# Kernel optimization log

Hardware: AMD Instinct MI355X
Metric: run time of the kernel (lower is better)

The kernel has to match this reference:

```python
import jax, jax.numpy as jnp
import numpy as np

NEG_SLOPE = 0.01  # F.leaky_relu default used in the original forward


def setup_inputs() -> dict:
    key = jax.random.key(0)
    ks = jax.random.split(key, 6)
    B, N, D = 2, 4096, 128
    s = 1.0 / np.sqrt(D)
    return {
        "embed_feat": jax.random.normal(ks[0], (B, N, D), jnp.float32),
        "predict_G": 1,
        "W_demand": jax.random.normal(ks[1], (D,), jnp.float32) * s,
        "b_demand": jnp.zeros((1,), jnp.float32),
        "Wa": jax.random.normal(ks[2], (D, D), jnp.float32) * s,
        "w_l": jax.random.normal(ks[3], (D,), jnp.float32) * s,
        "w_r": jax.random.normal(ks[4], (D,), jnp.float32) * s,
    }


def reference(embed_feat, predict_G, W_demand, b_demand, Wa, w_l, w_r):
    # demands: sigmoid(Linear(D->1)) -> [B, N]
    demands = jax.nn.sigmoid(embed_feat @ W_demand + b_demand[0])
    if not predict_G:
        return (demands, None)
    # proj = Wa(x): [B, N, D]  (torch Linear: x @ Wa.T)
    proj = jnp.einsum('bnd,ed->bne', embed_feat, Wa)
    # per-node scalar scores; A[b,i,j] = l[b,i] + r[b,j] (vectorized form of the O(N^2) loop)
    l = proj @ w_l  # [B, N]
    r = proj @ w_r  # [B, N]
    A = jax.nn.leaky_relu(l[:, :, None] + r[:, None, :], negative_slope=NEG_SLOPE)
    # original softmax over dim=1 of [N, N, 1] == over j axis
    Q = jax.nn.softmax(A, axis=2)  # [B, N, N]
    # rel_Ds[b,i,j] = demands[b,i]
    Gs = Q * demands[:, :, None]
    return (demands, Gs)
```

## Files before the change

kernel.cpp:

```cpp
#include <hip/hip_runtime.h>
#include <stdint.h>

#define N 4096
#define B 2
#define D 128
#define LOG2E 1.4426950408889634f

__device__ __forceinline__ float lrelu(float t) { return t > 0.f ? t : 0.01f * t; }

__global__ __launch_bounds__(256) void k1_uvec(
    const float* __restrict__ Wa,
    const float* __restrict__ w_l,
    const float* __restrict__ w_r,
    float* __restrict__ u) {
    __shared__ float2 pl[4][64];
    __shared__ float2 pr[4][64];
    int t = threadIdx.x;
    int d2 = t & 63;
    int h = t >> 6;
    const float2* Wa2 = (const float2*)Wa;
    float2 al = make_float2(0.f, 0.f), ar = make_float2(0.f, 0.f);
    #pragma unroll 8
    for (int k = 0; k < 32; ++k) {
        int e = h * 32 + k;
        float2 w = Wa2[e * 64 + d2];
        float wl = w_l[e];
        float wr = w_r[e];
        al.x += w.x * wl; al.y += w.y * wl;
        ar.x += w.x * wr; ar.y += w.y * wr;
    }
    pl[h][d2] = al; pr[h][d2] = ar;
    __syncthreads();
    if (t < 64) {
        float2 s = make_float2(0.f, 0.f);
        #pragma unroll
        for (int hh = 0; hh < 4; ++hh) { s.x += pl[hh][t].x; s.y += pl[hh][t].y; }
        ((float2*)u)[t] = s;
    } else if (t < 128) {
        int dd = t - 64;
        float2 s = make_float2(0.f, 0.f);
        #pragma unroll
        for (int hh = 0; hh < 4; ++hh) { s.x += pr[hh][dd].x; s.y += pr[hh][dd].y; }
        ((float2*)(u + D))[dd] = s;
    }
}

__global__ __launch_bounds__(256) void k2_rows(
    const float* __restrict__ x,
    const float* __restrict__ Wd,
    const float* __restrict__ bd,
    const float* __restrict__ u,
    float* __restrict__ out_dem,
    float* __restrict__ lv,
    float* __restrict__ rv) {
    int lane = threadIdx.x & 63;
    int row = blockIdx.x * 4 + (threadIdx.x >> 6);
    float2 xv = ((const float2*)(x + (size_t)row * D))[lane];
    float2 ul2 = ((const float2*)u)[lane];
    float2 ur2 = ((const float2*)(u + D))[lane];
    float2 wv = ((const float2*)Wd)[lane];
    float pl = xv.x * ul2.x + xv.y * ul2.y;
    float pr = xv.x * ur2.x + xv.y * ur2.y;
    float pd = xv.x * wv.x + xv.y * wv.y;
    #pragma unroll
    for (int m = 32; m >= 1; m >>= 1) {
        pl += __shfl_xor(pl, m, 64);
        pr += __shfl_xor(pr, m, 64);
        pd += __shfl_xor(pd, m, 64);
    }
    if (lane == 0) {
        float dem = 1.f / (1.f + __expf(-(pd + bd[0])));
        out_dem[row] = dem;
        lv[row] = pl * LOG2E;
        rv[row] = pr * LOG2E;
    }
}

__global__ __launch_bounds__(256) void k3_main(
    const float* __restrict__ lv, const float* __restrict__ rv,
    const float* __restrict__ dem_f,
    float* __restrict__ out_g) {
    __shared__ float sr[N];
    __shared__ float redmax[4];
    __shared__ float redsum[4][4];
    int tid = threadIdx.x;
    int b = blockIdx.x >> 10;
    int i0 = (blockIdx.x & 1023) << 2;
    const float* rb = rv + b * N;
    float lmax = -3.402823466e38f;
    #pragma unroll
    for (int k = 0; k < N / 256; ++k) {
        float v = rb[tid + k * 256];
        sr[tid + k * 256] = v;
        lmax = fmaxf(lmax, v);
    }
    #pragma unroll
    for (int m = 32; m >= 1; m >>= 1) lmax = fmaxf(lmax, __shfl_xor(lmax, m, 64));
    if ((tid & 63) == 0) redmax[tid >> 6] = lmax;
    __syncthreads();
    float rmax = fmaxf(fmaxf(redmax[0], redmax[1]), fmaxf(redmax[2], redmax[3]));

    int rowbase = b * N + i0;
    float lr_[4], mr[4], s[4];
    #pragma unroll
    for (int q = 0; q < 4; ++q) {
        lr_[q] = lv[rowbase + q];
        mr[q] = lrelu(lr_[q] + rmax);
        s[q] = 0.f;
    }
    #pragma unroll 2
    for (int k = 0; k < N / 256; ++k) {
        float r = sr[tid + k * 256];
        #pragma unroll
        for (int q = 0; q < 4; ++q) s[q] += exp2f(lrelu(lr_[q] + r) - mr[q]);
    }
    #pragma unroll
    for (int m = 32; m >= 1; m >>= 1) {
        #pragma unroll
        for (int q = 0; q < 4; ++q) s[q] += __shfl_xor(s[q], m, 64);
    }
    if ((tid & 63) == 0) {
        #pragma unroll
        for (int q = 0; q < 4; ++q) redsum[tid >> 6][q] = s[q];
    }
    __syncthreads();
    float sc[4];
    #pragma unroll
    for (int q = 0; q < 4; ++q) {
        float den = redsum[0][q] + redsum[1][q] + redsum[2][q] + redsum[3][q];
        sc[q] = dem_f[rowbase + q] / den;
    }
    const float4* rb4 = (const float4*)rb;
    size_t gbase = (size_t)b * N * N + (size_t)i0 * N;
    #pragma unroll
    for (int it = 0; it < 4; ++it) {
        int idx = it * 256 + tid;
        float4 r4 = rb4[idx];
        #pragma unroll
        for (int q = 0; q < 4; ++q) {
            float4 o;
            o.x = exp2f(lrelu(lr_[q] + r4.x) - mr[q]) * sc[q];
            o.y = exp2f(lrelu(lr_[q] + r4.y) - mr[q]) * sc[q];
            o.z = exp2f(lrelu(lr_[q] + r4.z) - mr[q]) * sc[q];
            o.w = exp2f(lrelu(lr_[q] + r4.w) - mr[q]) * sc[q];
            *(float4*)(out_g + gbase + (size_t)q * N + (size_t)idx * 4) = o;
        }
    }
}

extern "C" void kernel_launch(void* const* d_in, const int* in_sizes, int n_in,
                              void* d_out, int out_size, void* d_ws, size_t ws_size,
                              hipStream_t stream) {
    const float* x  = (const float*)d_in[0];
    const float* Wd = (const float*)d_in[2];
    const float* bd = (const float*)d_in[3];
    const float* Wa = (const float*)d_in[4];
    const float* wl = (const float*)d_in[5];
    const float* wr = (const float*)d_in[6];

    float* ws = (float*)d_ws;
    float* u  = ws;
    float* lv = ws + 256;
    float* rv = ws + 256 + 8192;

    float* out     = (float*)d_out;
    float* out_dem = out;
    float* out_g   = out + B * N;

    hipLaunchKernelGGL(k1_uvec, dim3(1), dim3(256), 0, stream, Wa, wl, wr, u);
    hipLaunchKernelGGL(k2_rows, dim3(B * N / 4), dim3(256), 0, stream,
                       x, Wd, bd, u, out_dem, lv, rv);
    hipLaunchKernelGGL(k3_main, dim3(B * N / 4), dim3(256), 0, stream,
                       lv, rv, out_dem, out_g);
}
```

Baseline: 155.7 us.

## Factor softmax exponentials into per-column precomputed terms and global max

The leaky-relu softmax exponent is split into exp2(l+r) for positive and exp2(0.01(l+r)) for negative arguments, each factored into a per-row scale times a per-column term. A new kernel precomputes exp2(r-rmax) and exp2(0.01(r-rmax)) per column, and the per-batch max of r is found once with an ordered-integer atomicMax instead of in every block. The main kernel then needs only compares, selects and multiplies with no per-element exp2, and its stores are nontemporal. The costs are an extra launch, four times more column data read per block, and possible overflow or precision loss when the factored terms are far from the max.

```diff
diff --git a/kernel.cpp b/kernel.cpp
--- a/kernel.cpp
+++ b/kernel.cpp
@@ -6,16 +6,28 @@
 #define D 128
 #define LOG2E 1.4426950408889634f
 
+typedef float f32x4 __attribute__((ext_vector_type(4)));
+
 __device__ __forceinline__ float lrelu(float t) { return t > 0.f ? t : 0.01f * t; }
+
+__device__ __forceinline__ unsigned f2ord(float f) {
+    unsigned u = __float_as_uint(f);
+    return (u & 0x80000000u) ? ~u : (u | 0x80000000u);
+}
+__device__ __forceinline__ float ord2f(unsigned o) {
+    return __uint_as_float((o & 0x80000000u) ? (o ^ 0x80000000u) : ~o);
+}
 
 __global__ __launch_bounds__(256) void k1_uvec(
     const float* __restrict__ Wa,
     const float* __restrict__ w_l,
     const float* __restrict__ w_r,
-    float* __restrict__ u) {
+    float* __restrict__ u,
+    unsigned* __restrict__ gmax) {
     __shared__ float2 pl[4][64];
     __shared__ float2 pr[4][64];
     int t = threadIdx.x;
+    if (t < B) gmax[t] = 0u;
     int d2 = t & 63;
     int h = t >> 6;
     const float2* Wa2 = (const float2*)Wa;
@@ -52,7 +64,8 @@
     const float* __restrict__ u,
     float* __restrict__ out_dem,
     float* __restrict__ lv,
-    float* __restrict__ rv) {
+    float4* __restrict__ q4,
+    unsigned* __restrict__ gmax) {
     int lane = threadIdx.x & 63;
     int row = blockIdx.x * 4 + (threadIdx.x >> 6);
     float2 xv = ((const float2*)(x + (size_t)row * D))[lane];
@@ -72,78 +85,95 @@
         float dem = 1.f / (1.f + __expf(-(pd + bd[0])));
         out_dem[row] = dem;
         lv[row] = pl * LOG2E;
-        rv[row] = pr * LOG2E;
-    }
+        float r = pr * LOG2E;
+        q4[row].x = r;
+        atomicMax(gmax + (row >> 12), f2ord(r));
+    }
+}
+
+__global__ __launch_bounds__(256) void k2b_fpm(
+    float4* __restrict__ q4,
+    const unsigned* __restrict__ gmax) {
+    int j = blockIdx.x * 256 + threadIdx.x;
+    float rmax = ord2f(gmax[j >> 12]);
+    float r = q4[j].x;
+    float t = r - rmax;
+    q4[j] = make_float4(r, exp2f(t), exp2f(0.01f * t), 0.f);
 }
 
 __global__ __launch_bounds__(256) void k3_main(
-    const float* __restrict__ lv, const float* __restrict__ rv,
+    const float* __restrict__ lv,
+    const float4* __restrict__ q4,
+    const unsigned* __restrict__ gmax,
     const float* __restrict__ dem_f,
     float* __restrict__ out_g) {
-    __shared__ float sr[N];
-    __shared__ float redmax[4];
-    __shared__ float redsum[4][4];
+    __shared__ float red[4][8];
     int tid = threadIdx.x;
     int b = blockIdx.x >> 10;
     int i0 = (blockIdx.x & 1023) << 2;
-    const float* rb = rv + b * N;
-    float lmax = -3.402823466e38f;
-    #pragma unroll
+    const float4* qb = q4 + (size_t)b * N;
+    float rmax = ord2f(gmax[b]);
+    int rowbase = b * N + i0;
+
+    float l_[4];
+    #pragma unroll
+    for (int q = 0; q < 4; ++q) l_[q] = lv[rowbase + q];
+
+    float s1[4] = {0.f, 0.f, 0.f, 0.f}, s2[4] = {0.f, 0.f, 0.f, 0.f};
+    #pragma unroll 4
     for (int k = 0; k < N / 256; ++k) {
-        float v = rb[tid + k * 256];
-        sr[tid + k * 256] = v;
-        lmax = fmaxf(lmax, v);
-    }
-    #pragma unroll
-    for (int m = 32; m >= 1; m >>= 1) lmax = fmaxf(lmax, __shfl_xor(lmax, m, 64));
-    if ((tid & 63) == 0) redmax[tid >> 6] = lmax;
+        float4 v = qb[tid + k * 256];
+        #pragma unroll
+        for (int q = 0; q < 4; ++q) {
+            bool pos = (l_[q] + v.x) > 0.f;
+            s1[q] += pos ? v.y : 0.f;
+            s2[q] += pos ? 0.f : v.z;
+        }
+    }
+    #pragma unroll
+    for (int m = 32; m >= 1; m >>= 1) {
+        #pragma unroll
+        for (int q = 0; q < 4; ++q) {
+            s1[q] += __shfl_xor(s1[q], m, 64);
+            s2[q] += __shfl_xor(s2[q], m, 64);
+        }
+    }
+    int w = tid >> 6;
+    if ((tid & 63) == 0) {
+        #pragma unroll
+        for (int q = 0; q < 4; ++q) { red[w][q] = s1[q]; red[w][4 + q] = s2[q]; }
+    }
     __syncthreads();
-    float rmax = fmaxf(fmaxf(redmax[0], redmax[1]), fmaxf(redmax[2], redmax[3]));
-
-    int rowbase = b * N + i0;
-    float lr_[4], mr[4], s[4];
+    float eP[4], eM[4];
     #pragma unroll
     for (int q = 0; q < 4; ++q) {
-        lr_[q] = lv[rowbase + q];
-        mr[q] = lrelu(lr_[q] + rmax);
-        s[q] = 0.f;
-    }
-    #pragma unroll 2
-    for (int k = 0; k < N / 256; ++k) {
-        float r = sr[tid + k * 256];
-        #pragma unroll
-        for (int q = 0; q < 4; ++q) s[q] += exp2f(lrelu(lr_[q] + r) - mr[q]);
-    }
-    #pragma unroll
-    for (int m = 32; m >= 1; m >>= 1) {
-        #pragma unroll
-        for (int q = 0; q < 4; ++q) s[q] += __shfl_xor(s[q], m, 64);
-    }
-    if ((tid & 63) == 0) {
-        #pragma unroll
-        for (int q = 0; q < 4; ++q) redsum[tid >> 6][q] = s[q];
-    }
-    __syncthreads();
-    float sc[4];
-    #pragma unroll
-    for (int q = 0; q < 4; ++q) {
-        float den = redsum[0][q] + redsum[1][q] + redsum[2][q] + redsum[3][q];
-        sc[q] = dem_f[rowbase + q] / den;
-    }
-    const float4* rb4 = (const float4*)rb;
+        float S1 = red[0][q] + red[1][q] + red[2][q] + red[3][q];
+        float S2 = red[0][4 + q] + red[1][4 + q] + red[2][4 + q] + red[3][4 + q];
+        float t0 = l_[q] + rmax;
+        float m0 = lrelu(t0);
+        float Ep = exp2f(t0 - m0);
+        float Em = exp2f(0.01f * t0 - m0);
+        float sc = dem_f[rowbase + q] / (Ep * S1 + Em * S2);
+        eP[q] = Ep * sc;
+        eM[q] = Em * sc;
+    }
+
     size_t gbase = (size_t)b * N * N + (size_t)i0 * N;
     #pragma unroll
     for (int it = 0; it < 4; ++it) {
         int idx = it * 256 + tid;
-        float4 r4 = rb4[idx];
+        float4 v0 = qb[idx * 4 + 0];
+        float4 v1 = qb[idx * 4 + 1];
+        float4 v2 = qb[idx * 4 + 2];
+        float4 v3 = qb[idx * 4 + 3];
         #pragma unroll
         for (int q = 0; q < 4; ++q) {
-            float4 o;
-            o.x = exp2f(lrelu(lr_[q] + r4.x) - mr[q]) * sc[q];
-            o.y = exp2f(lrelu(lr_[q] + r4.y) - mr[q]) * sc[q];
-            o.z = exp2f(lrelu(lr_[q] + r4.z) - mr[q]) * sc[q];
-            o.w = exp2f(lrelu(lr_[q] + r4.w) - mr[q]) * sc[q];
-            *(float4*)(out_g + gbase + (size_t)q * N + (size_t)idx * 4) = o;
+            f32x4 o;
+            o.x = (l_[q] + v0.x > 0.f) ? eP[q] * v0.y : eM[q] * v0.z;
+            o.y = (l_[q] + v1.x > 0.f) ? eP[q] * v1.y : eM[q] * v1.z;
+            o.z = (l_[q] + v2.x > 0.f) ? eP[q] * v2.y : eM[q] * v2.z;
+            o.w = (l_[q] + v3.x > 0.f) ? eP[q] * v3.y : eM[q] * v3.z;
+            __builtin_nontemporal_store(o, (f32x4*)(out_g + gbase + (size_t)q * N) + idx);
         }
     }
 }
@@ -161,15 +191,17 @@
     float* ws = (float*)d_ws;
     float* u  = ws;
     float* lv = ws + 256;
-    float* rv = ws + 256 + 8192;
+    float4* q4 = (float4*)(ws + 256 + 8192);
+    unsigned* gmax = (unsigned*)(ws + 256 + 8192 + 4 * 8192);
 
     float* out     = (float*)d_out;
     float* out_dem = out;
     float* out_g   = out + B * N;
 
-    hipLaunchKernelGGL(k1_uvec, dim3(1), dim3(256), 0, stream, Wa, wl, wr, u);
+    hipLaunchKernelGGL(k1_uvec, dim3(1), dim3(256), 0, stream, Wa, wl, wr, u, gmax);
     hipLaunchKernelGGL(k2_rows, dim3(B * N / 4), dim3(256), 0, stream,
-                       x, Wd, bd, u, out_dem, lv, rv);
+                       x, Wd, bd, u, out_dem, lv, q4, gmax);
+    hipLaunchKernelGGL(k2b_fpm, dim3(B * N / 256), dim3(256), 0, stream, q4, gmax);
     hipLaunchKernelGGL(k3_main, dim3(B * N / 4), dim3(256), 0, stream,
-                       lv, rv, out_dem, out_g);
-}
+                       lv, q4, gmax, out_dem, out_g);
+}
```

After: 259.4 us. +66.5%, slower.

## Fuse all stages into one cooperative kernel with factored leaky-relu exponentials

Applied to the files above, without the earlier changes.

Merges the three kernels into one cooperative launch of 512 blocks with a grid-wide sync between the per-row projection stage and the softmax stage. Each block now handles 16 rows instead of 4, and every block recomputes the tiny Wa·w vectors itself. The exp2 of leaky_relu(l+r) is factored into per-column tables exp2(r-rmax) and exp2(0.01(r-rmax)) held in LDS, selected per element by a threshold compare. This removes the per-element transcendental from the output loop. The cost is a grid sync, redundant per-block Wa work, a register-heavy 16-row store loop, and dependence on cooperative-launch residency.

```diff
diff --git a/kernel.cpp b/kernel.cpp
--- a/kernel.cpp
+++ b/kernel.cpp
@@ -1,149 +1,167 @@
 #include <hip/hip_runtime.h>
+#include <hip/hip_cooperative_groups.h>
 #include <stdint.h>
+
+namespace cg = cooperative_groups;
 
 #define N 4096
 #define B 2
 #define D 128
 #define LOG2E 1.4426950408889634f
 
+typedef float f32x4 __attribute__((ext_vector_type(4)));
+
 __device__ __forceinline__ float lrelu(float t) { return t > 0.f ? t : 0.01f * t; }
 
-__global__ __launch_bounds__(256) void k1_uvec(
+__global__ __launch_bounds__(256, 2) void kfused(
+    const float* __restrict__ x,
+    const float* __restrict__ Wd,
+    const float* __restrict__ bd,
     const float* __restrict__ Wa,
     const float* __restrict__ w_l,
     const float* __restrict__ w_r,
-    float* __restrict__ u) {
-    __shared__ float2 pl[4][64];
-    __shared__ float2 pr[4][64];
+    float* __restrict__ colR,
+    float* __restrict__ out_dem,
+    float* __restrict__ out_g) {
+    __shared__ float sFp[N];
+    __shared__ float sFm[N];
+    __shared__ float uLR[2][D];
+    __shared__ float sWd[D];
+    __shared__ float redm[4];
+    __shared__ float4 rowfacS[16];
+
     int t = threadIdx.x;
-    int d2 = t & 63;
-    int h = t >> 6;
-    const float2* Wa2 = (const float2*)Wa;
-    float2 al = make_float2(0.f, 0.f), ar = make_float2(0.f, 0.f);
-    #pragma unroll 8
-    for (int k = 0; k < 32; ++k) {
-        int e = h * 32 + k;
-        float2 w = Wa2[e * 64 + d2];
-        float wl = w_l[e];
-        float wr = w_r[e];
-        al.x += w.x * wl; al.y += w.y * wl;
-        ar.x += w.x * wr; ar.y += w.y * wr;
-    }
-    pl[h][d2] = al; pr[h][d2] = ar;
-    __syncthreads();
-    if (t < 64) {
-        float2 s = make_float2(0.f, 0.f);
-        #pragma unroll
-        for (int hh = 0; hh < 4; ++hh) { s.x += pl[hh][t].x; s.y += pl[hh][t].y; }
-        ((float2*)u)[t] = s;
-    } else if (t < 128) {
-        int dd = t - 64;
-        float2 s = make_float2(0.f, 0.f);
-        #pragma unroll
-        for (int hh = 0; hh < 4; ++hh) { s.x += pr[hh][dd].x; s.y += pr[hh][dd].y; }
-        ((float2*)(u + D))[dd] = s;
-    }
-}
+    int lane = t & 63;
+    int w = t >> 6;
+    int bk = blockIdx.x;
+    int row0 = bk << 4;
+    int b = bk >> 8;
 
-__global__ __launch_bounds__(256) void k2_rows(
-    const float* __restrict__ x,
-    const float* __restrict__ Wd,
-    const float* __restrict__ bd,
-    const float* __restrict__ u,
-    float* __restrict__ out_dem,
-    float* __restrict__ lv,
-    float* __restrict__ rv) {
-    int lane = threadIdx.x & 63;
-    int row = blockIdx.x * 4 + (threadIdx.x >> 6);
-    float2 xv = ((const float2*)(x + (size_t)row * D))[lane];
-    float2 ul2 = ((const float2*)u)[lane];
-    float2 ur2 = ((const float2*)(u + D))[lane];
-    float2 wv = ((const float2*)Wd)[lane];
-    float pl = xv.x * ul2.x + xv.y * ul2.y;
-    float pr = xv.x * ur2.x + xv.y * ur2.y;
-    float pd = xv.x * wv.x + xv.y * wv.y;
-    #pragma unroll
-    for (int m = 32; m >= 1; m >>= 1) {
-        pl += __shfl_xor(pl, m, 64);
-        pr += __shfl_xor(pr, m, 64);
-        pd += __shfl_xor(pd, m, 64);
-    }
-    if (lane == 0) {
-        float dem = 1.f / (1.f + __expf(-(pd + bd[0])));
-        out_dem[row] = dem;
-        lv[row] = pl * LOG2E;
-        rv[row] = pr * LOG2E;
-    }
-}
-
-__global__ __launch_bounds__(256) void k3_main(
-    const float* __restrict__ lv, const float* __restrict__ rv,
-    const float* __restrict__ dem_f,
-    float* __restrict__ out_g) {
-    __shared__ float sr[N];
-    __shared__ float redmax[4];
-    __shared__ float redsum[4][4];
-    int tid = threadIdx.x;
-    int b = blockIdx.x >> 10;
-    int i0 = (blockIdx.x & 1023) << 2;
-    const float* rb = rv + b * N;
-    float lmax = -3.402823466e38f;
-    #pragma unroll
-    for (int k = 0; k < N / 256; ++k) {
-        float v = rb[tid + k * 256];
-        sr[tid + k * 256] = v;
-        lmax = fmaxf(lmax, v);
-    }
-    #pragma unroll
-    for (int m = 32; m >= 1; m >>= 1) lmax = fmaxf(lmax, __shfl_xor(lmax, m, 64));
-    if ((tid & 63) == 0) redmax[tid >> 6] = lmax;
-    __syncthreads();
-    float rmax = fmaxf(fmaxf(redmax[0], redmax[1]), fmaxf(redmax[2], redmax[3]));
-
-    int rowbase = b * N + i0;
-    float lr_[4], mr[4], s[4];
-    #pragma unroll
-    for (int q = 0; q < 4; ++q) {
-        lr_[q] = lv[rowbase + q];
-        mr[q] = lrelu(lr_[q] + rmax);
-        s[q] = 0.f;
-    }
-    #pragma unroll 2
-    for (int k = 0; k < N / 256; ++k) {
-        float r = sr[tid + k * 256];
-        #pragma unroll
-        for (int q = 0; q < 4; ++q) s[q] += exp2f(lrelu(lr_[q] + r) - mr[q]);
-    }
-    #pragma unroll
-    for (int m = 32; m >= 1; m >>= 1) {
-        #pragma unroll
-        for (int q = 0; q < 4; ++q) s[q] += __shfl_xor(s[q], m, 64);
-    }
-    if ((tid & 63) == 0) {
-        #pragma unroll
-        for (int q = 0; q < 4; ++q) redsum[tid >> 6][q] = s[q];
+    {
+        int d = t & 127;
+        int sel = t >> 7;
+        const float* wv = sel ? w_r : w_l;
+        float acc = 0.f;
+        #pragma unroll 8
+        for (int e = 0; e < 128; ++e)
+            acc += Wa[e * 128 + d] * wv[e];
+        uLR[sel][d] = acc;
+        if (t < 128) sWd[t] = Wd[t];
     }
     __syncthreads();
-    float sc[4];
+
+    float lq[4], demq[4];
+    {
+        float2 ul2 = ((const float2*)uLR[0])[lane];
+        float2 ur2 = ((const float2*)uLR[1])[lane];
+        float2 wd2 = ((const float2*)sWd)[lane];
+        #pragma unroll
+        for (int rr = 0; rr < 4; ++rr) {
+            int row = row0 + w * 4 + rr;
+            float2 xv = ((const float2*)(x + (size_t)row * D))[lane];
+            float pl = xv.x * ul2.x + xv.y * ul2.y;
+            float pr = xv.x * ur2.x + xv.y * ur2.y;
+            float pd = xv.x * wd2.x + xv.y * wd2.y;
+            #pragma unroll
+            for (int m = 32; m >= 1; m >>= 1) {
+                pl += __shfl_xor(pl, m, 64);
+                pr += __shfl_xor(pr, m, 64);
+                pd += __shfl_xor(pd, m, 64);
+            }
+            demq[rr] = 1.f / (1.f + __expf(-(pd + bd[0])));
+            lq[rr] = pl * LOG2E;
+            if (lane == 0) {
+                out_dem[row] = demq[rr];
+                colR[row] = pr * LOG2E;
+            }
+        }
+    }
+    __threadfence();
+    cg::this_grid().sync();
+
+    float rloc[16];
+    {
+        const float* rb = colR + ((size_t)b << 12);
+        float m = -3.402823466e38f;
+        #pragma unroll
+        for (int k = 0; k < 16; ++k) {
+            rloc[k] = rb[t + k * 256];
+            m = fmaxf(m, rloc[k]);
+        }
+        #pragma unroll
+        for (int s = 32; s >= 1; s >>= 1) m = fmaxf(m, __shfl_xor(m, s, 64));
+        if (lane == 0) redm[w] = m;
+    }
+    __syncthreads();
+    float rmax = fmaxf(fmaxf(redm[0], redm[1]), fmaxf(redm[2], redm[3]));
     #pragma unroll
-    for (int q = 0; q < 4; ++q) {
-        float den = redsum[0][q] + redsum[1][q] + redsum[2][q] + redsum[3][q];
-        sc[q] = dem_f[rowbase + q] / den;
+    for (int k = 0; k < 16; ++k) {
+        float dd = rloc[k] - rmax;
+        sFp[t + k * 256] = exp2f(dd);
+        sFm[t + k * 256] = exp2f(0.01f * dd);
     }
-    const float4* rb4 = (const float4*)rb;
-    size_t gbase = (size_t)b * N * N + (size_t)i0 * N;
+    __syncthreads();
+
+    {
+        float thr[4];
+        #pragma unroll
+        for (int rr = 0; rr < 4; ++rr) thr[rr] = exp2f(-(lq[rr] + rmax));
+        float s1[4] = {0.f, 0.f, 0.f, 0.f}, s2[4] = {0.f, 0.f, 0.f, 0.f};
+        #pragma unroll 4
+        for (int k = 0; k < 16; ++k) {
+            int idx = lane + k * 64;
+            float4 fp = ((const float4*)sFp)[idx];
+            float4 fm = ((const float4*)sFm)[idx];
+            #pragma unroll
+            for (int rr = 0; rr < 4; ++rr) {
+                bool p0 = fp.x > thr[rr]; s1[rr] += p0 ? fp.x : 0.f; s2[rr] += p0 ? 0.f : fm.x;
+                bool p1 = fp.y > thr[rr]; s1[rr] += p1 ? fp.y : 0.f; s2[rr] += p1 ? 0.f : fm.y;
+                bool p2 = fp.z > thr[rr]; s1[rr] += p2 ? fp.z : 0.f; s2[rr] += p2 ? 0.f : fm.z;
+                bool p3 = fp.w > thr[rr]; s1[rr] += p3 ? fp.w : 0.f; s2[rr] += p3 ? 0.f : fm.w;
+            }
+        }
+        #pragma unroll
+        for (int s = 32; s >= 1; s >>= 1) {
+            #pragma unroll
+            for (int rr = 0; rr < 4; ++rr) {
+                s1[rr] += __shfl_xor(s1[rr], s, 64);
+                s2[rr] += __shfl_xor(s2[rr], s, 64);
+            }
+        }
+        if (lane == 0) {
+            #pragma unroll
+            for (int rr = 0; rr < 4; ++rr) {
+                float t0 = lq[rr] + rmax;
+                float m0 = lrelu(t0);
+                float Ep = exp2f(t0 - m0);
+                float Em = exp2f(0.01f * t0 - m0);
+                float sc = demq[rr] / (Ep * s1[rr] + Em * s2[rr]);
+                rowfacS[w * 4 + rr] = make_float4(thr[rr], Ep * sc, Em * sc, 0.f);
+            }
+        }
+    }
+    __syncthreads();
+
+    float thv[16], ePv[16], eMv[16];
+    #pragma unroll
+    for (int ri = 0; ri < 16; ++ri) {
+        float4 rf = rowfacS[ri];
+        thv[ri] = rf.x; ePv[ri] = rf.y; eMv[ri] = rf.z;
+    }
+    f32x4* outp = (f32x4*)out_g + ((size_t)row0 << 10);
     #pragma unroll
     for (int it = 0; it < 4; ++it) {
-        int idx = it * 256 + tid;
-        float4 r4 = rb4[idx];
+        int idx = it * 256 + t;
+        float4 fp = ((const float4*)sFp)[idx];
+        float4 fm = ((const float4*)sFm)[idx];
         #pragma unroll
-        for (int q = 0; q < 4; ++q) {
-            float4 o;
-            o.x = exp2f(lrelu(lr_[q] + r4.x) - mr[q]) * sc[q];
-            o.y = exp2f(lrelu(lr_[q] + r4.y) - mr[q]) * sc[q];
-            o.z = exp2f(lrelu(lr_[q] + r4.z) - mr[q]) * sc[q];
-            o.w = exp2f(lrelu(lr_[q] + r4.w) - mr[q]) * sc[q];
-            *(float4*)(out_g + gbase + (size_t)q * N + (size_t)idx * 4) = o;
+        for (int ri = 0; ri < 16; ++ri) {
+            f32x4 o;
+            o.x = fp.x > thv[ri] ? ePv[ri] * fp.x : eMv[ri] * fm.x;
+            o.y = fp.y > thv[ri] ? ePv[ri] * fp.y : eMv[ri] * fm.y;
+            o.z = fp.z > thv[ri] ? ePv[ri] * fp.z : eMv[ri] * fm.z;
+            o.w = fp.w > thv[ri] ? ePv[ri] * fp.w : eMv[ri] * fm.w;
+            outp[((size_t)ri << 10) + idx] = o;
         }
     }
 }
@@ -158,18 +176,14 @@
     const float* wl = (const float*)d_in[5];
     const float* wr = (const float*)d_in[6];
 
-    float* ws = (float*)d_ws;
-    float* u  = ws;
-    float* lv = ws + 256;
-    float* rv = ws + 256 + 8192;
+    float* colR = (float*)d_ws;
 
     float* out     = (float*)d_out;
     float* out_dem = out;
     float* out_g   = out + B * N;
 
-    hipLaunchKernelGGL(k1_uvec, dim3(1), dim3(256), 0, stream, Wa, wl, wr, u);
-    hipLaunchKernelGGL(k2_rows, dim3(B * N / 4), dim3(256), 0, stream,
-                       x, Wd, bd, u, out_dem, lv, rv);
-    hipLaunchKernelGGL(k3_main, dim3(B * N / 4), dim3(256), 0, stream,
-                       lv, rv, out_dem, out_g);
+    void* args[] = {(void*)&x, (void*)&Wd, (void*)&bd, (void*)&Wa, (void*)&wl,
+                    (void*)&wr, (void*)&colR, (void*)&out_dem, (void*)&out_g};
+    hipLaunchCooperativeKernel((const void*)kfused, dim3(512), dim3(256),
+                               args, 0, stream);
 }
```

Result: slower. 235.2 us (+51.0%).
